# Kernel optimization log

Measured on AMD Instinct MI355X. Metric: run time of the kernel, lower is better.

The kernel has to match this reference:

```python
import jax, jax.numpy as jnp
import numpy as np

B, S, D = 4, 2048, 1024
NH, NKV = 16, 4
HD = D // NH  # 64


def _rope(x, freqs):
    # x: [B, H, S, HD], freqs: [B, S, HD//2]
    cos = jnp.concatenate([jnp.cos(freqs), jnp.cos(freqs)], axis=-1)[:, None]  # [B,1,S,HD]
    sin = jnp.concatenate([jnp.sin(freqs), jnp.sin(freqs)], axis=-1)[:, None]
    x1, x2 = x[..., : HD // 2], x[..., HD // 2:]
    rot = jnp.concatenate([-x2, x1], axis=-1)
    return x * cos + rot * sin


def setup_inputs() -> dict:
    key = jax.random.key(0)
    ks = jax.random.split(key, 9)
    return {
        "hidden_states": jax.random.normal(ks[0], (B, S, D), jnp.float32),
        "rotary_pos_emb": jax.random.normal(ks[1], (B, S, HD // 2), jnp.float32),
        "Wq": jax.random.normal(ks[2], (D, NH * HD), jnp.float32) * 0.02,
        "bq": jax.random.normal(ks[3], (NH * HD,), jnp.float32) * 0.02,
        "Wk": jax.random.normal(ks[4], (D, NKV * HD), jnp.float32) * 0.02,
        "bk": jax.random.normal(ks[5], (NKV * HD,), jnp.float32) * 0.02,
        "Wv": jax.random.normal(ks[6], (D, NKV * HD), jnp.float32) * 0.02,
        "bv": jax.random.normal(ks[7], (NKV * HD,), jnp.float32) * 0.02,
        "Wo": jax.random.normal(ks[8], (NH * HD, D), jnp.float32) * 0.02,
    }


def reference(hidden_states, rotary_pos_emb, Wq, bq, Wk, bk, Wv, bv, Wo):
    b, s, _ = hidden_states.shape
    # projections -> [B, H, S, HD]
    q = (hidden_states @ Wq + bq).reshape(b, s, NH, HD).transpose(0, 2, 1, 3)
    k = (hidden_states @ Wk + bk).reshape(b, s, NKV, HD).transpose(0, 2, 1, 3)
    v = (hidden_states @ Wv + bv).reshape(b, s, NKV, HD).transpose(0, 2, 1, 3)
    q = _rope(q, rotary_pos_emb)
    k = _rope(k, rotary_pos_emb)
    groups = NH // NKV
    k = jnp.repeat(k, groups, axis=1)  # [B, NH, S, HD]
    v = jnp.repeat(v, groups, axis=1)
    scaling = HD ** -0.5
    scores = jnp.einsum("bhqd,bhkd->bhqk", q, k) * scaling
    probs = jax.nn.softmax(scores.astype(jnp.float32), axis=-1).astype(q.dtype)
    out = jnp.einsum("bhqk,bhkd->bhqd", probs, v)
    out = out.transpose(0, 2, 1, 3).reshape(b, s, NH * HD)
    return out @ Wo
```

## Files before the change

kernel.cpp:

```cpp
#include <hip/hip_runtime.h>
#include <hip/hip_bf16.h>

#define BB 4
#define SS 2048
#define DD 1024
#define NH 16
#define NKV 4
#define HD 64
#define MROWS (BB*SS)
#define NQKV (NH*HD + 2*NKV*HD)
#define KOFF (NH*HD)

typedef short v8s __attribute__((ext_vector_type(8)));
typedef short v4s __attribute__((ext_vector_type(4)));
typedef float v4f __attribute__((ext_vector_type(4)));
typedef unsigned short u16;
typedef unsigned int u32;

__device__ __forceinline__ float bf2f(u16 u){
  union { float f; u32 i; } x; x.i = ((u32)u) << 16; return x.f;
}
__device__ __forceinline__ u16 f2bf(float f){
  union { __hip_bfloat16 h; u16 u; } x; x.h = __float2bfloat16(f); return x.u;
}
__device__ __forceinline__ u32 cvtpk(float lo, float hi){
  u32 r;
  asm("v_cvt_pk_bf16_f32 %0, %1, %2" : "=v"(r) : "v"(lo), "v"(hi));
  return r;
}
__device__ __forceinline__ v4f vmax4(v4f a, v4f b){
  v4f r;
  #pragma unroll
  for (int j=0;j<4;j++) r[j] = fmaxf(a[j], b[j]);
  return r;
}
__device__ __forceinline__ void gl_lds16(const u16* g, u16* l){
  __builtin_amdgcn_global_load_lds(
      (const __attribute__((address_space(1))) u32*)g,
      (__attribute__((address_space(3))) u32*)l, 16, 0, 0);
}


__global__ void cast_x(const float* __restrict__ in, u16* __restrict__ out, int n4){
  int i = blockIdx.x*256 + threadIdx.x;
  if (i >= n4) return;
  float4 v = reinterpret_cast<const float4*>(in)[i];
  ushort4 o;
  o.x = f2bf(v.x); o.y = f2bf(v.y); o.z = f2bf(v.z); o.w = f2bf(v.w);
  reinterpret_cast<ushort4*>(out)[i] = o;
}

__global__ void build_bqkv(const float* __restrict__ Wq, const float* __restrict__ Wk,
                           const float* __restrict__ Wv, const float* __restrict__ bq,
                           const float* __restrict__ bk, const float* __restrict__ bv,
                           u16* __restrict__ Bt, float* __restrict__ bias){
  int idx = blockIdx.x*256 + threadIdx.x;
  int n = idx >> 10, k = idx & 1023;
  float v;
  if (n < 1024)      v = Wq[k*1024 + n];
  else if (n < 1280) v = Wk[k*256 + (n-1024)];
  else               v = Wv[k*256 + (n-1280)];
  Bt[idx] = f2bf(v);
  if (k == 0) bias[n] = (n < 1024) ? bq[n] : (n < 1280 ? bk[n-1024] : bv[n-1280]);
}

__global__ void build_wo(const float* __restrict__ Wo, u16* __restrict__ Bt){
  int idx = blockIdx.x*256 + threadIdx.x;
  int n = idx >> 10, k = idx & 1023;
  Bt[idx] = f2bf(Wo[k*1024 + n]);
}

__global__ void rope_k(u16* __restrict__ QKV, const float* __restrict__ fr){
  int idx = blockIdx.x*256 + threadIdx.x;
  int d  = idx & 31;
  int hh = (idx >> 5) & 3;
  long row = idx >> 7;
  int col = KOFF + hh*HD + d;
  u16* p = QKV + row*NQKV;
  float x1 = bf2f(p[col]);
  float x2 = bf2f(p[col+32]);
  float f = fr[row*32 + d];
  float sn, cs; __sincosf(f, &sn, &cs);
  p[col]    = f2bf(x1*cs - x2*sn);
  p[col+32] = f2bf(x2*cs + x1*sn);
}


template<bool BIAS, typename OT>
__global__ __launch_bounds__(256) void gemm_bt(
    const u16* __restrict__ A, const u16* __restrict__ Bt,
    const float* __restrict__ bias, OT* __restrict__ C,
    int K, int ldc)
{
  __shared__ u16 As[128*32];
  __shared__ u16 Bs[128*32];
  const int tid = threadIdx.x;
  const int wid = tid >> 6, lane = tid & 63;
  const int g = lane >> 4, c = lane & 15;
  const long brow = (long)blockIdx.y * 128;
  const long bcol = (long)blockIdx.x * 128;
  const int wr = (wid >> 1) * 64, wc = (wid & 1) * 64;
  const int srow = tid >> 2;
  const int scol = (tid & 3) * 8;
  const u16* ga = &A [(brow + srow)*K + scol];
  const u16* gb = &Bt[(bcol + srow)*K + scol];
  u16* la = &As[(wid*64)*8];
  u16* lb = &Bs[(wid*64)*8];
  v4f acc[4][4] = {};
  for (int kt = 0; kt < K; kt += 32) {
    __syncthreads();
    gl_lds16(ga + kt,          la);
    gl_lds16(ga + 64*K + kt,   la + 256*8);
    gl_lds16(gb + kt,          lb);
    gl_lds16(gb + 64*K + kt,   lb + 256*8);
    __syncthreads();
    v8s af[4], bf[4];
    #pragma unroll
    for (int m=0;m<4;m++) af[m] = *reinterpret_cast<const v8s*>(&As[(wr + m*16 + c)*32 + g*8]);
    #pragma unroll
    for (int n=0;n<4;n++) bf[n] = *reinterpret_cast<const v8s*>(&Bs[(wc + n*16 + c)*32 + g*8]);
    __builtin_amdgcn_s_setprio(1);
    #pragma unroll
    for (int m=0;m<4;m++)
      #pragma unroll
      for (int n=0;n<4;n++)
        acc[m][n] = __builtin_amdgcn_mfma_f32_16x16x32_bf16(af[m], bf[n], acc[m][n], 0,0,0);
    __builtin_amdgcn_s_setprio(0);
  }
  #pragma unroll
  for (int m=0;m<4;m++)
    #pragma unroll
    for (int n=0;n<4;n++) {
      int col = (int)bcol + wc + n*16 + c;
      float badd = BIAS ? bias[col] : 0.0f;
      #pragma unroll
      for (int r2=0;r2<4;r2++){
        long row = brow + wr + m*16 + g*4 + r2;
        float v = acc[m][n][r2] + badd;
        if constexpr (sizeof(OT)==2) C[row*ldc + col] = (OT)f2bf(v);
        else                         C[row*ldc + col] = (OT)v;
      }
    }
}


__global__ __launch_bounds__(512) void attn_k(const u16* __restrict__ QKV,
                                              const float* __restrict__ fr,
                                              u16* __restrict__ Out){
  __shared__ u16 Ks[2][64][72];
  __shared__ u16 Vs[2][64][72];
  const int tid = threadIdx.x;
  const int wid = tid >> 6, lane = tid & 63;
  const int g = lane >> 4, c = lane & 15;
  const int qt = blockIdx.x & 7;
  const int bh = blockIdx.x >> 3;
  const int b = bh >> 4, h = bh & 15;
  const int kvh = h >> 2;
  const u16* Qb = QKV + (long)b*SS*NQKV + h*HD;
  const u16* Kb = QKV + (long)b*SS*NQKV + KOFF + kvh*HD;
  const u16* Vb = Kb + NKV*HD;

  const float SCL = 0.125f * 1.44269504088896f;
  v8s qf[2][2];
  #pragma unroll
  for (int qn=0;qn<2;qn++){
    int lrow = qt*256 + wid*32 + qn*16 + c;
    v8s q0 = *reinterpret_cast<const v8s*>(&Qb[(long)lrow*NQKV + g*8]);
    v8s q1 = *reinterpret_cast<const v8s*>(&Qb[(long)lrow*NQKV + 32 + g*8]);
    const float* frp = fr + ((long)b*SS + lrow)*32 + g*8;
    float4 f0 = *reinterpret_cast<const float4*>(frp);
    float4 f1 = *reinterpret_cast<const float4*>(frp + 4);
    float fa[8] = {f0.x,f0.y,f0.z,f0.w,f1.x,f1.y,f1.z,f1.w};
    float r0[8], r1[8];
    #pragma unroll
    for (int j=0;j<8;j++){
      float x1 = bf2f((u16)q0[j]), x2 = bf2f((u16)q1[j]);
      float sn, cs; __sincosf(fa[j], &sn, &cs);
      r0[j] = (x1*cs - x2*sn) * SCL;
      r1[j] = (x2*cs + x1*sn) * SCL;
    }
    union { v8s v; u32 w[4]; } a0, a1;
    #pragma unroll
    for (int wi=0;wi<4;wi++){
      a0.w[wi] = cvtpk(r0[2*wi], r0[2*wi+1]);
      a1.w[wi] = cvtpk(r1[2*wi], r1[2*wi+1]);
    }
    qf[qn][0] = a0.v; qf[qn][1] = a1.v;
  }

  v8s onesf;
  {
    short ov = (c==0) ? (short)0x3F80 : (short)0;
    #pragma unroll
    for (int j=0;j<8;j++) onesf[j] = ov;
  }

  v4f o[2][5] = {};
  float mr[2] = {-1e30f, -1e30f};

  const int krow = tid >> 3;
  const int kcol = (tid & 7) * 8;
  const int key0 = 2*(tid >> 4);
  const int dg4  = (tid & 15) * 4;
  const int slot0 = 32*(key0>>5) + 8*((key0>>2)&3) + 4*((key0>>4)&1) + (key0&3);
  int vofs[4];
  #pragma unroll
  for (int j=0;j<4;j++){
    int d = dg4 + j;
    int idx = (((slot0>>3) ^ (d>>3)) << 3) | (slot0 & 7);
    vofs[j] = d*72 + idx;
  }
  u16* VsF = &Vs[0][0][0];

  const u16* kp  = Kb + (long)krow*NQKV + kcol;
  const u16* vp0 = Vb + (long)key0*NQKV + dg4;
  const u16* vp1 = vp0 + NQKV;

  v8s kreg;
  union { v4s v; u32 w[2]; } vr0, vr1;

  {
    kreg  = *reinterpret_cast<const v8s*>(kp);
    vr0.v = *reinterpret_cast<const v4s*>(vp0);
    vr1.v = *reinterpret_cast<const v4s*>(vp1);
    *reinterpret_cast<v8s*>(&Ks[0][krow][kcol]) = kreg;
    #pragma unroll
    for (int j=0;j<4;j++){
      u32 pkd = __builtin_amdgcn_perm(vr1.w[j>>1], vr0.w[j>>1],
                                      (j&1) ? 0x07060302u : 0x05040100u);
      *reinterpret_cast<u32*>(&VsF[vofs[j]]) = pkd;
    }
  }
  __syncthreads();

  int p = 0;
  for (int t = 0; t < SS/64; ++t){
    if (t+1 < SS/64) {
      long off = (long)(t+1)*64*NQKV;
      kreg  = *reinterpret_cast<const v8s*>(kp  + off);
      vr0.v = *reinterpret_cast<const v4s*>(vp0 + off);
      vr1.v = *reinterpret_cast<const v4s*>(vp1 + off);
    }

    v4f st[4][2] = {};
    #pragma unroll
    for (int ks=0;ks<2;ks++){
      v8s kf[4];
      #pragma unroll
      for (int km=0;km<4;km++)
        kf[km] = *reinterpret_cast<const v8s*>(&Ks[p][km*16 + c][ks*32 + g*8]);
      __builtin_amdgcn_s_setprio(1);
      #pragma unroll
      for (int km=0;km<4;km++)
        #pragma unroll
        for (int qn=0;qn<2;qn++)
          st[km][qn] = __builtin_amdgcn_mfma_f32_16x16x32_bf16(kf[km], qf[qn][ks], st[km][qn], 0,0,0);
      __builtin_amdgcn_s_setprio(0);
    }

    float al[2];
    bool upd[2];
    #pragma unroll
    for (int qn=0;qn<2;qn++){
      v4f m4 = vmax4(vmax4(st[0][qn], st[1][qn]), vmax4(st[2][qn], st[3][qn]));
      float mx = fmaxf(fmaxf(m4[0], m4[1]), fmaxf(m4[2], m4[3]));
      upd[qn] = !__all(mx <= mr[qn] + 8.0f);
      al[qn] = 1.0f;
      if (upd[qn]) {
        mx = fmaxf(mx, __shfl_xor(mx, 16));
        mx = fmaxf(mx, __shfl_xor(mx, 32));
        float nm = fmaxf(mr[qn], mx);
        al[qn] = __builtin_amdgcn_exp2f(mr[qn] - nm);
        mr[qn] = nm;
      }
      #pragma unroll
      for (int km=0;km<4;km++)
        #pragma unroll
        for (int r2=0;r2<4;r2++)
          st[km][qn][r2] = __builtin_amdgcn_exp2f(st[km][qn][r2] - mr[qn]);
    }

    v8s pa[2][2];
    #pragma unroll
    for (int qm=0;qm<2;qm++)
      #pragma unroll
      for (int ks=0;ks<2;ks++){
        union { v8s v; u32 w[4]; } u;
        u.w[0] = cvtpk(st[2*ks  ][qm][0], st[2*ks  ][qm][1]);
        u.w[1] = cvtpk(st[2*ks  ][qm][2], st[2*ks  ][qm][3]);
        u.w[2] = cvtpk(st[2*ks+1][qm][0], st[2*ks+1][qm][1]);
        u.w[3] = cvtpk(st[2*ks+1][qm][2], st[2*ks+1][qm][3]);
        pa[qm][ks] = u.v;
      }

    if (upd[0] | upd[1]) {
      #pragma unroll
      for (int qm=0;qm<2;qm++)
        #pragma unroll
        for (int r2=0;r2<4;r2++){
          float a = __shfl(al[qm], g*4 + r2);
          #pragma unroll
          for (int dn=0;dn<5;dn++) o[qm][dn][r2] *= a;
        }
    }

    #pragma unroll
    for (int ks=0;ks<2;ks++){
      __builtin_amdgcn_s_setprio(1);
      #pragma unroll
      for (int dn=0;dn<4;dn++){
        int d0 = dn*16 + c;
        v8s vf = *reinterpret_cast<const v8s*>(&Vs[p][d0][(((ks*4+g) ^ (d0>>3)) << 3)]);
        #pragma unroll
        for (int qm=0;qm<2;qm++)
          o[qm][dn] = __builtin_amdgcn_mfma_f32_16x16x32_bf16(pa[qm][ks], vf, o[qm][dn], 0,0,0);
      }
      #pragma unroll
      for (int qm=0;qm<2;qm++)
        o[qm][4] = __builtin_amdgcn_mfma_f32_16x16x32_bf16(pa[qm][ks], onesf, o[qm][4], 0,0,0);
      __builtin_amdgcn_s_setprio(0);
    }

    if (t+1 < SS/64) {
      *reinterpret_cast<v8s*>(&Ks[p^1][krow][kcol]) = kreg;
      const int bofs = (p^1) * (64*72);
      #pragma unroll
      for (int j=0;j<4;j++){
        u32 pkd = __builtin_amdgcn_perm(vr1.w[j>>1], vr0.w[j>>1],
                                        (j&1) ? 0x07060302u : 0x05040100u);
        *reinterpret_cast<u32*>(&VsF[bofs + vofs[j]]) = pkd;
      }
    }
    __syncthreads();
    p ^= 1;
  }

  #pragma unroll
  for (int qm=0;qm<2;qm++)
    #pragma unroll
    for (int r2=0;r2<4;r2++){
      float l = __shfl(o[qm][4][r2], lane & 48);
      float inv = 1.0f / l;
      long row = (long)b*SS + qt*256 + wid*32 + qm*16 + g*4 + r2;
      #pragma unroll
      for (int dn=0;dn<4;dn++)
        Out[row*DD + h*HD + dn*16 + c] = f2bf(o[qm][dn][r2] * inv);
    }
}


extern "C" void kernel_launch(void* const* d_in, const int* in_sizes, int n_in,
                              void* d_out, int out_size, void* d_ws, size_t ws_size,
                              hipStream_t stream)
{
  const float* hs = (const float*)d_in[0];
  const float* fr = (const float*)d_in[1];
  const float* Wq = (const float*)d_in[2];
  const float* bq = (const float*)d_in[3];
  const float* Wk = (const float*)d_in[4];
  const float* bk = (const float*)d_in[5];
  const float* Wv = (const float*)d_in[6];
  const float* bv = (const float*)d_in[7];
  const float* Wo = (const float*)d_in[8];
  float* out = (float*)d_out;
  char* ws = (char*)d_ws;

  u16*   Xb   = (u16*)(ws);
  u16*   Bqkv = (u16*)(ws + 16777216);
  u16*   WoT  = (u16*)(ws + 16777216 + 3145728);
  float* bias = (float*)(ws + 16777216 + 3145728 + 2097152);
  u16*   QKV  = (u16*)(ws + 22028288);
  u16*   AO   = (u16*)(ws + 22028288 + 25165824);

  cast_x   <<<8192, 256, 0, stream>>>(hs, Xb, MROWS*DD/4);
  build_bqkv<<<6144, 256, 0, stream>>>(Wq, Wk, Wv, bq, bk, bv, Bqkv, bias);
  build_wo <<<4096, 256, 0, stream>>>(Wo, WoT);
  gemm_bt<true,  u16>  <<<dim3(NQKV/128, MROWS/128), 256, 0, stream>>>(Xb, Bqkv, bias, QKV, DD, NQKV);
  rope_k   <<<MROWS*NKV*32/256, 256, 0, stream>>>(QKV, fr);
  attn_k   <<<BB*NH*(SS/256), 512, 0, stream>>>(QKV, fr, AO);
  gemm_bt<false, float><<<dim3(DD/128, MROWS/128), 256, 0, stream>>>(AO, WoT, nullptr, out, DD, DD);
}
```

Baseline: 184.4 us.

## Shrink attention blocks to 256 threads and fold max subtraction into MFMA init

The attention kernel now uses 256-thread blocks covering 128 query rows, which doubles the grid and gives each thread twice as many K/V staging loads per tile. The V tile pad changes to 76, with 8 d-rows per thread. Scores are now initialised with the negated running max so the MFMA accumulates the shifted logits directly, removing a subtraction per element before exp2. The max reduction uses three-input max trees. Smaller blocks should improve scheduling flexibility, but each K/V tile is now loaded by twice as many blocks, which adds L2 traffic.

```diff
diff --git a/kernel.cpp b/kernel.cpp
--- a/kernel.cpp
+++ b/kernel.cpp
@@ -10,6 +10,7 @@
 #define MROWS (BB*SS)
 #define NQKV (NH*HD + 2*NKV*HD)
 #define KOFF (NH*HD)
+#define VPAD 76
 
 typedef short v8s __attribute__((ext_vector_type(8)));
 typedef short v4s __attribute__((ext_vector_type(4)));
@@ -28,11 +29,8 @@
   asm("v_cvt_pk_bf16_f32 %0, %1, %2" : "=v"(r) : "v"(lo), "v"(hi));
   return r;
 }
-__device__ __forceinline__ v4f vmax4(v4f a, v4f b){
-  v4f r;
-  #pragma unroll
-  for (int j=0;j<4;j++) r[j] = fmaxf(a[j], b[j]);
-  return r;
+__device__ __forceinline__ float fmax3(float a, float b, float c){
+  return fmaxf(fmaxf(a, b), c);
 }
 __device__ __forceinline__ void gl_lds16(const u16* g, u16* l){
   __builtin_amdgcn_global_load_lds(
@@ -144,16 +142,16 @@
 }
 
 
-__global__ __launch_bounds__(512) void attn_k(const u16* __restrict__ QKV,
+__global__ __launch_bounds__(256) void attn_k(const u16* __restrict__ QKV,
                                               const float* __restrict__ fr,
                                               u16* __restrict__ Out){
   __shared__ u16 Ks[2][64][72];
-  __shared__ u16 Vs[2][64][72];
+  __shared__ u16 Vs[2][64][VPAD];
   const int tid = threadIdx.x;
   const int wid = tid >> 6, lane = tid & 63;
   const int g = lane >> 4, c = lane & 15;
-  const int qt = blockIdx.x & 7;
-  const int bh = blockIdx.x >> 3;
+  const int qt = blockIdx.x & 15;
+  const int bh = blockIdx.x >> 4;
   const int b = bh >> 4, h = bh & 15;
   const int kvh = h >> 2;
   const u16* Qb = QKV + (long)b*SS*NQKV + h*HD;
@@ -164,7 +162,7 @@
   v8s qf[2][2];
   #pragma unroll
   for (int qn=0;qn<2;qn++){
-    int lrow = qt*256 + wid*32 + qn*16 + c;
+    int lrow = qt*128 + wid*32 + qn*16 + c;
     v8s q0 = *reinterpret_cast<const v8s*>(&Qb[(long)lrow*NQKV + g*8]);
     v8s q1 = *reinterpret_cast<const v8s*>(&Qb[(long)lrow*NQKV + 32 + g*8]);
     const float* frp = fr + ((long)b*SS + lrow)*32 + g*8;
@@ -196,39 +194,37 @@
   }
 
   v4f o[2][5] = {};
-  float mr[2] = {-1e30f, -1e30f};
-
-  const int krow = tid >> 3;
-  const int kcol = (tid & 7) * 8;
-  const int key0 = 2*(tid >> 4);
-  const int dg4  = (tid & 15) * 4;
+  float mr[2] = {0.f, 0.f};
+
+  const int ksrow = tid >> 3;
+  const int kscol = (tid & 7) * 8;
+  const int key0  = 2*(tid >> 3);
+  const int dg    = tid & 7;
   const int slot0 = 32*(key0>>5) + 8*((key0>>2)&3) + 4*((key0>>4)&1) + (key0&3);
-  int vofs[4];
-  #pragma unroll
-  for (int j=0;j<4;j++){
-    int d = dg4 + j;
-    int idx = (((slot0>>3) ^ (d>>3)) << 3) | (slot0 & 7);
-    vofs[j] = d*72 + idx;
-  }
+  const int idx0  = (((slot0>>3) ^ dg) << 3) | (slot0 & 7);
+  const int vbase = (dg*8)*VPAD + idx0;
   u16* VsF = &Vs[0][0][0];
 
-  const u16* kp  = Kb + (long)krow*NQKV + kcol;
-  const u16* vp0 = Vb + (long)key0*NQKV + dg4;
+  const u16* kp0 = Kb + (long)ksrow*NQKV + kscol;
+  const u16* kp1 = kp0 + 32*NQKV;
+  const u16* vp0 = Vb + (long)key0*NQKV + dg*8;
   const u16* vp1 = vp0 + NQKV;
 
-  v8s kreg;
-  union { v4s v; u32 w[2]; } vr0, vr1;
+  v8s kreg0, kreg1;
+  union { v8s v; u32 w[4]; } vr0, vr1;
 
   {
-    kreg  = *reinterpret_cast<const v8s*>(kp);
-    vr0.v = *reinterpret_cast<const v4s*>(vp0);
-    vr1.v = *reinterpret_cast<const v4s*>(vp1);
-    *reinterpret_cast<v8s*>(&Ks[0][krow][kcol]) = kreg;
-    #pragma unroll
-    for (int j=0;j<4;j++){
+    kreg0 = *reinterpret_cast<const v8s*>(kp0);
+    kreg1 = *reinterpret_cast<const v8s*>(kp1);
+    vr0.v = *reinterpret_cast<const v8s*>(vp0);
+    vr1.v = *reinterpret_cast<const v8s*>(vp1);
+    *reinterpret_cast<v8s*>(&Ks[0][ksrow][kscol])    = kreg0;
+    *reinterpret_cast<v8s*>(&Ks[0][32+ksrow][kscol]) = kreg1;
+    #pragma unroll
+    for (int j=0;j<8;j++){
       u32 pkd = __builtin_amdgcn_perm(vr1.w[j>>1], vr0.w[j>>1],
                                       (j&1) ? 0x07060302u : 0x05040100u);
-      *reinterpret_cast<u32*>(&VsF[vofs[j]]) = pkd;
+      *reinterpret_cast<u32*>(&VsF[vbase + j*VPAD]) = pkd;
     }
   }
   __syncthreads();
@@ -237,12 +233,19 @@
   for (int t = 0; t < SS/64; ++t){
     if (t+1 < SS/64) {
       long off = (long)(t+1)*64*NQKV;
-      kreg  = *reinterpret_cast<const v8s*>(kp  + off);
-      vr0.v = *reinterpret_cast<const v4s*>(vp0 + off);
-      vr1.v = *reinterpret_cast<const v4s*>(vp1 + off);
-    }
-
-    v4f st[4][2] = {};
+      kreg0 = *reinterpret_cast<const v8s*>(kp0 + off);
+      kreg1 = *reinterpret_cast<const v8s*>(kp1 + off);
+      vr0.v = *reinterpret_cast<const v8s*>(vp0 + off);
+      vr1.v = *reinterpret_cast<const v8s*>(vp1 + off);
+    }
+
+    v4f st[4][2];
+    #pragma unroll
+    for (int qn=0;qn<2;qn++){
+      v4f mi = {-mr[qn], -mr[qn], -mr[qn], -mr[qn]};
+      #pragma unroll
+      for (int km=0;km<4;km++) st[km][qn] = mi;
+    }
     #pragma unroll
     for (int ks=0;ks<2;ks++){
       v8s kf[4];
@@ -262,22 +265,31 @@
     bool upd[2];
     #pragma unroll
     for (int qn=0;qn<2;qn++){
-      v4f m4 = vmax4(vmax4(st[0][qn], st[1][qn]), vmax4(st[2][qn], st[3][qn]));
-      float mx = fmaxf(fmaxf(m4[0], m4[1]), fmaxf(m4[2], m4[3]));
-      upd[qn] = !__all(mx <= mr[qn] + 8.0f);
+      float t0 = fmax3(st[0][qn][0], st[0][qn][1], st[0][qn][2]);
+      float t1 = fmax3(st[0][qn][3], st[1][qn][0], st[1][qn][1]);
+      float t2 = fmax3(st[1][qn][2], st[1][qn][3], st[2][qn][0]);
+      float t3 = fmax3(st[2][qn][1], st[2][qn][2], st[2][qn][3]);
+      float t4 = fmax3(st[3][qn][0], st[3][qn][1], st[3][qn][2]);
+      float mx = fmaxf(fmax3(t0, t1, t2), fmax3(t3, t4, st[3][qn][3]));
+      upd[qn] = !__all(mx <= 8.0f);
       al[qn] = 1.0f;
       if (upd[qn]) {
         mx = fmaxf(mx, __shfl_xor(mx, 16));
         mx = fmaxf(mx, __shfl_xor(mx, 32));
-        float nm = fmaxf(mr[qn], mx);
-        al[qn] = __builtin_amdgcn_exp2f(mr[qn] - nm);
-        mr[qn] = nm;
+        float d = fmaxf(mx, 0.0f);
+        al[qn] = __builtin_amdgcn_exp2f(-d);
+        mr[qn] += d;
+        #pragma unroll
+        for (int km=0;km<4;km++)
+          #pragma unroll
+          for (int r2=0;r2<4;r2++)
+            st[km][qn][r2] -= d;
       }
       #pragma unroll
       for (int km=0;km<4;km++)
         #pragma unroll
         for (int r2=0;r2<4;r2++)
-          st[km][qn][r2] = __builtin_amdgcn_exp2f(st[km][qn][r2] - mr[qn]);
+          st[km][qn][r2] = __builtin_amdgcn_exp2f(st[km][qn][r2]);
     }
 
     v8s pa[2][2];
@@ -322,13 +334,14 @@
     }
 
     if (t+1 < SS/64) {
-      *reinterpret_cast<v8s*>(&Ks[p^1][krow][kcol]) = kreg;
-      const int bofs = (p^1) * (64*72);
-      #pragma unroll
-      for (int j=0;j<4;j++){
+      *reinterpret_cast<v8s*>(&Ks[p^1][ksrow][kscol])    = kreg0;
+      *reinterpret_cast<v8s*>(&Ks[p^1][32+ksrow][kscol]) = kreg1;
+      const int bofs = (p^1) * (64*VPAD);
+      #pragma unroll
+      for (int j=0;j<8;j++){
         u32 pkd = __builtin_amdgcn_perm(vr1.w[j>>1], vr0.w[j>>1],
                                         (j&1) ? 0x07060302u : 0x05040100u);
-        *reinterpret_cast<u32*>(&VsF[bofs + vofs[j]]) = pkd;
+        *reinterpret_cast<u32*>(&VsF[bofs + vbase + j*VPAD]) = pkd;
       }
     }
     __syncthreads();
@@ -341,7 +354,7 @@
     for (int r2=0;r2<4;r2++){
       float l = __shfl(o[qm][4][r2], lane & 48);
       float inv = 1.0f / l;
-      long row = (long)b*SS + qt*256 + wid*32 + qm*16 + g*4 + r2;
+      long row = (long)b*SS + qt*128 + wid*32 + qm*16 + g*4 + r2;
       #pragma unroll
       for (int dn=0;dn<4;dn++)
         Out[row*DD + h*HD + dn*16 + c] = f2bf(o[qm][dn][r2] * inv);
@@ -377,6 +390,6 @@
   build_wo <<<4096, 256, 0, stream>>>(Wo, WoT);
   gemm_bt<true,  u16>  <<<dim3(NQKV/128, MROWS/128), 256, 0, stream>>>(Xb, Bqkv, bias, QKV, DD, NQKV);
   rope_k   <<<MROWS*NKV*32/256, 256, 0, stream>>>(QKV, fr);
-  attn_k   <<<BB*NH*(SS/256), 512, 0, stream>>>(QKV, fr, AO);
+  attn_k   <<<BB*NH*(SS/128), 256, 0, stream>>>(QKV, fr, AO);
   gemm_bt<false, float><<<dim3(DD/128, MROWS/128), 256, 0, stream>>>(AO, WoT, nullptr, out, DD, DD);
 }
```

Result: slower. 201.0 us (+9.0%).

## Double GEMM K-tile to 64 and fold running max into attention score accumulator

Applied to the files above, without the earlier changes.

The projection GEMM now loads a 64-wide K slice per iteration instead of 32, which halves the number of barrier pairs and doubles the MFMA work between synchronisations, at the cost of twice the LDS footprint. In the attention kernel, the score accumulators are initialised with the negated running max so the MFMA yields scores already shifted, removing a per-element subtraction in the common no-update path. The max reduction uses three-input fmax chains. The initial running max changes from a large negative value to zero, which alters the rescaling logic and could affect numerics for very negative scores.

```diff
diff --git a/kernel.cpp b/kernel.cpp
--- a/kernel.cpp
+++ b/kernel.cpp
@@ -28,11 +28,8 @@
   asm("v_cvt_pk_bf16_f32 %0, %1, %2" : "=v"(r) : "v"(lo), "v"(hi));
   return r;
 }
-__device__ __forceinline__ v4f vmax4(v4f a, v4f b){
-  v4f r;
-  #pragma unroll
-  for (int j=0;j<4;j++) r[j] = fmaxf(a[j], b[j]);
-  return r;
+__device__ __forceinline__ float fmax3(float a, float b, float c){
+  return fmaxf(fmaxf(a, b), c);
 }
 __device__ __forceinline__ void gl_lds16(const u16* g, u16* l){
   __builtin_amdgcn_global_load_lds(
@@ -92,40 +89,44 @@
     const float* __restrict__ bias, OT* __restrict__ C,
     int K, int ldc)
 {
-  __shared__ u16 As[128*32];
-  __shared__ u16 Bs[128*32];
+  __shared__ u16 As[128*64];
+  __shared__ u16 Bs[128*64];
   const int tid = threadIdx.x;
   const int wid = tid >> 6, lane = tid & 63;
   const int g = lane >> 4, c = lane & 15;
   const long brow = (long)blockIdx.y * 128;
   const long bcol = (long)blockIdx.x * 128;
   const int wr = (wid >> 1) * 64, wc = (wid & 1) * 64;
-  const int srow = tid >> 2;
-  const int scol = (tid & 3) * 8;
+  const int srow = tid >> 3;
+  const int scol = (tid & 7) * 8;
   const u16* ga = &A [(brow + srow)*K + scol];
   const u16* gb = &Bt[(bcol + srow)*K + scol];
-  u16* la = &As[(wid*64)*8];
-  u16* lb = &Bs[(wid*64)*8];
+  u16* la = &As[(wid*8)*64];
+  u16* lb = &Bs[(wid*8)*64];
   v4f acc[4][4] = {};
-  for (int kt = 0; kt < K; kt += 32) {
+  for (int kt = 0; kt < K; kt += 64) {
     __syncthreads();
-    gl_lds16(ga + kt,          la);
-    gl_lds16(ga + 64*K + kt,   la + 256*8);
-    gl_lds16(gb + kt,          lb);
-    gl_lds16(gb + 64*K + kt,   lb + 256*8);
+    #pragma unroll
+    for (int e = 0; e < 4; ++e) {
+      gl_lds16(ga + (long)e*32*K + kt, la + e*32*64);
+      gl_lds16(gb + (long)e*32*K + kt, lb + e*32*64);
+    }
     __syncthreads();
-    v8s af[4], bf[4];
-    #pragma unroll
-    for (int m=0;m<4;m++) af[m] = *reinterpret_cast<const v8s*>(&As[(wr + m*16 + c)*32 + g*8]);
-    #pragma unroll
-    for (int n=0;n<4;n++) bf[n] = *reinterpret_cast<const v8s*>(&Bs[(wc + n*16 + c)*32 + g*8]);
-    __builtin_amdgcn_s_setprio(1);
-    #pragma unroll
-    for (int m=0;m<4;m++)
-      #pragma unroll
-      for (int n=0;n<4;n++)
-        acc[m][n] = __builtin_amdgcn_mfma_f32_16x16x32_bf16(af[m], bf[n], acc[m][n], 0,0,0);
-    __builtin_amdgcn_s_setprio(0);
+    #pragma unroll
+    for (int ks = 0; ks < 2; ++ks) {
+      v8s af[4], bf[4];
+      #pragma unroll
+      for (int m=0;m<4;m++) af[m] = *reinterpret_cast<const v8s*>(&As[(wr + m*16 + c)*64 + ks*32 + g*8]);
+      #pragma unroll
+      for (int n=0;n<4;n++) bf[n] = *reinterpret_cast<const v8s*>(&Bs[(wc + n*16 + c)*64 + ks*32 + g*8]);
+      __builtin_amdgcn_s_setprio(1);
+      #pragma unroll
+      for (int m=0;m<4;m++)
+        #pragma unroll
+        for (int n=0;n<4;n++)
+          acc[m][n] = __builtin_amdgcn_mfma_f32_16x16x32_bf16(af[m], bf[n], acc[m][n], 0,0,0);
+      __builtin_amdgcn_s_setprio(0);
+    }
   }
   #pragma unroll
   for (int m=0;m<4;m++)
@@ -196,7 +197,7 @@
   }
 
   v4f o[2][5] = {};
-  float mr[2] = {-1e30f, -1e30f};
+  float mr[2] = {0.f, 0.f};
 
   const int krow = tid >> 3;
   const int kcol = (tid & 7) * 8;
@@ -242,7 +243,13 @@
       vr1.v = *reinterpret_cast<const v4s*>(vp1 + off);
     }
 
-    v4f st[4][2] = {};
+    v4f st[4][2];
+    #pragma unroll
+    for (int qn=0;qn<2;qn++){
+      v4f mi = {-mr[qn], -mr[qn], -mr[qn], -mr[qn]};
+      #pragma unroll
+      for (int km=0;km<4;km++) st[km][qn] = mi;
+    }
     #pragma unroll
     for (int ks=0;ks<2;ks++){
       v8s kf[4];
@@ -262,22 +269,31 @@
     bool upd[2];
     #pragma unroll
     for (int qn=0;qn<2;qn++){
-      v4f m4 = vmax4(vmax4(st[0][qn], st[1][qn]), vmax4(st[2][qn], st[3][qn]));
-      float mx = fmaxf(fmaxf(m4[0], m4[1]), fmaxf(m4[2], m4[3]));
-      upd[qn] = !__all(mx <= mr[qn] + 8.0f);
+      float t0 = fmax3(st[0][qn][0], st[0][qn][1], st[0][qn][2]);
+      float t1 = fmax3(st[0][qn][3], st[1][qn][0], st[1][qn][1]);
+      float t2 = fmax3(st[1][qn][2], st[1][qn][3], st[2][qn][0]);
+      float t3 = fmax3(st[2][qn][1], st[2][qn][2], st[2][qn][3]);
+      float t4 = fmax3(st[3][qn][0], st[3][qn][1], st[3][qn][2]);
+      float mx = fmaxf(fmax3(t0, t1, t2), fmax3(t3, t4, st[3][qn][3]));
+      upd[qn] = !__all(mx <= 8.0f);
       al[qn] = 1.0f;
       if (upd[qn]) {
         mx = fmaxf(mx, __shfl_xor(mx, 16));
         mx = fmaxf(mx, __shfl_xor(mx, 32));
-        float nm = fmaxf(mr[qn], mx);
-        al[qn] = __builtin_amdgcn_exp2f(mr[qn] - nm);
-        mr[qn] = nm;
+        float d = fmaxf(mx, 0.0f);
+        al[qn] = __builtin_amdgcn_exp2f(-d);
+        mr[qn] += d;
+        #pragma unroll
+        for (int km=0;km<4;km++)
+          #pragma unroll
+          for (int r2=0;r2<4;r2++)
+            st[km][qn][r2] -= d;
       }
       #pragma unroll
       for (int km=0;km<4;km++)
         #pragma unroll
         for (int r2=0;r2<4;r2++)
-          st[km][qn][r2] = __builtin_amdgcn_exp2f(st[km][qn][r2] - mr[qn]);
+          st[km][qn][r2] = __builtin_amdgcn_exp2f(st[km][qn][r2]);
     }
 
     v8s pa[2][2];
```

Result: faster. 177.4 us (-3.8%).
